# Kernel optimization log

Hardware: AMD Instinct MI355X
Metric: run time of the kernel (lower is better)

Reference implementation:

```python
import jax, jax.numpy as jnp
from jax import lax
import numpy as np

T = 3          # num_frame
DIV = 2        # channel_shift div
PAD = 1        # kernel_size//2 (same padding for k=3)


def setup_inputs() -> dict:
    key = jax.random.key(0)
    k1, k2 = jax.random.split(key)
    x = jax.random.normal(k1, (12, 64, 256, 256), dtype=jnp.float32)      # (B*T, C, H, W)
    weight = jax.random.normal(k2, (64, 64, 3, 3), dtype=jnp.float32)     # (O, I, kh, kw)
    return {"x": x, "weight": weight}


def reference(x, weight):
    BT, C, H, W = x.shape
    B = BT // T
    # channel_shift: view (B, T*C, H, W), roll by C//div along channel axis
    shift = C // DIV
    y = x.reshape(B, T * C, H, W)
    y = jnp.roll(y, shift, axis=1).reshape(BT, C, H, W)
    # BinaryConv2d: sign(activations), sign(weights) * per-out-channel mean|W|
    scale = jnp.mean(jnp.abs(weight), axis=(1, 2, 3), keepdims=True)      # (O,1,1,1)
    bw = jnp.sign(weight) * scale
    bx = jnp.sign(y)
    out = lax.conv_general_dilated(
        bx, bw,
        window_strides=(1, 1),
        padding=[(PAD, PAD), (PAD, PAD)],
        dimension_numbers=("NCHW", "OIHW", "NCHW"),
    )
    return out
```

## Files before the change

### kernel.cpp

```cpp
#include <hip/hip_runtime.h>
#include <stdint.h>

typedef unsigned long long u64;
typedef unsigned int u32;

#define HW 65536
#define WD 256

__global__ __launch_bounds__(64) void pack_w_kernel(const float* __restrict__ wt,
                                                    u64* __restrict__ pw,
                                                    float* __restrict__ scale) {
    const int o = blockIdx.x;
    const int i = threadIdx.x;
    const float* p = wt + o * 576 + i * 9;
    float v[9];
    float s = 0.f;
#pragma unroll
    for (int k = 0; k < 9; k++) { v[k] = p[k]; s += fabsf(v[k]); }
#pragma unroll
    for (int k = 0; k < 9; k++) {
        u64 m = __ballot((__float_as_uint(v[k]) >> 31) != 0u);
        if (i == 0) pw[o * 9 + k] = m;
    }
#pragma unroll
    for (int off = 32; off > 0; off >>= 1) s += __shfl_down(s, off);
    if (i == 0) scale[o] = s * (1.0f / 576.0f);
}

__global__ __launch_bounds__(256) void pack_x_kernel(const float* __restrict__ x,
                                                     u64* __restrict__ px) {
    const int n = blockIdx.x >> 6;
    const int s = ((blockIdx.x & 63) << 10) + (threadIdx.x << 2);
    const int b = n / 3;
    const int t = n - b * 3;
    const int fp = b * 3 + (t + 2) % 3;

    const float* xa = x + ((size_t)fp * 64 + 32) * HW + s;
    const float* xb = x + (size_t)n * 64 * HW + s;

    u32 lo0 = 0, lo1 = 0, lo2 = 0, lo3 = 0;
    u32 hi0 = 0, hi1 = 0, hi2 = 0, hi3 = 0;
#pragma unroll
    for (int c = 0; c < 32; c++) {
        float4 va = *(const float4*)(xa + (size_t)c * HW);
        lo0 |= (__float_as_uint(va.x) >> 31) << c;
        lo1 |= (__float_as_uint(va.y) >> 31) << c;
        lo2 |= (__float_as_uint(va.z) >> 31) << c;
        lo3 |= (__float_as_uint(va.w) >> 31) << c;
        float4 vb = *(const float4*)(xb + (size_t)c * HW);
        hi0 |= (__float_as_uint(vb.x) >> 31) << c;
        hi1 |= (__float_as_uint(vb.y) >> 31) << c;
        hi2 |= (__float_as_uint(vb.z) >> 31) << c;
        hi3 |= (__float_as_uint(vb.w) >> 31) << c;
    }
    u64* dst = px + (size_t)n * HW + s;
    dst[0] = ((u64)hi0 << 32) | lo0;
    dst[1] = ((u64)hi1 << 32) | lo1;
    dst[2] = ((u64)hi2 << 32) | lo2;
    dst[3] = ((u64)hi3 << 32) | lo3;
}

__global__ __launch_bounds__(256) void bconv_kernel(const u64* __restrict__ px,
                                                    const u64* __restrict__ pw,
                                                    const float* __restrict__ scale,
                                                    float* __restrict__ out) {
    const int w = (blockIdx.x << 6) + (threadIdx.x & 63);
    const int h = (blockIdx.y << 2) + (threadIdx.x >> 6);
    const int n = blockIdx.z;
    const u64* base = px + (size_t)n * HW;

    const bool edge_block = (blockIdx.x == 0) | (blockIdx.x == 3) |
                            (blockIdx.y == 0) | (blockIdx.y == 63);

    u64 xv[9];
    float* op = out + (size_t)n * 64 * HW + h * WD + w;

    if (!edge_block) {
#pragma unroll
        for (int dh = -1; dh <= 1; dh++)
#pragma unroll
            for (int dw = -1; dw <= 1; dw++)
                xv[(dh + 1) * 3 + (dw + 1)] = base[(h + dh) * WD + (w + dw)];

#pragma unroll 4
        for (int o = 0; o < 64; o++) {
            const u64* wp = pw + o * 9;
            int cnt = 0;
#pragma unroll
            for (int k = 0; k < 9; k++) cnt += __popcll(xv[k] ^ wp[k]);
            const float sc = scale[o];
            __builtin_nontemporal_store(fmaf(-2.f * sc, (float)cnt, 576.f * sc),
                                        op + (size_t)o * HW);
        }
    } else {
        u64 mk[9];
        int ninv = 0;
#pragma unroll
        for (int dh = -1; dh <= 1; dh++) {
#pragma unroll
            for (int dw = -1; dw <= 1; dw++) {
                const int k = (dh + 1) * 3 + (dw + 1);
                const int hh = h + dh, ww = w + dw;
                const bool valid = (hh >= 0) && (hh < 256) && (ww >= 0) && (ww < 256);
                const int hc = min(max(hh, 0), 255);
                const int wc = min(max(ww, 0), 255);
                xv[k] = base[hc * WD + wc];
                mk[k] = valid ? ~0ull : 0ull;
                ninv += valid ? 0 : 1;
            }
        }
        const int basecnt = 32 * ninv;

#pragma unroll 4
        for (int o = 0; o < 64; o++) {
            const u64* wp = pw + o * 9;
            int cnt = basecnt;
#pragma unroll
            for (int k = 0; k < 9; k++) cnt += __popcll((xv[k] ^ wp[k]) & mk[k]);
            const float sc = scale[o];
            __builtin_nontemporal_store(fmaf(-2.f * sc, (float)cnt, 576.f * sc),
                                        op + (size_t)o * HW);
        }
    }
}

extern "C" void kernel_launch(void* const* d_in, const int* in_sizes, int n_in,
                              void* d_out, int out_size, void* d_ws, size_t ws_size,
                              hipStream_t stream) {
    (void)in_sizes; (void)n_in; (void)out_size; (void)ws_size;
    const float* x  = (const float*)d_in[0];
    const float* wt = (const float*)d_in[1];
    float* out = (float*)d_out;

    u64* px = (u64*)d_ws;
    u64* pw = px + (size_t)12 * HW;
    float* scale = (float*)(pw + 576);

    pack_w_kernel<<<64, 64, 0, stream>>>(wt, pw, scale);
    pack_x_kernel<<<768, 256, 0, stream>>>(x, px);
    bconv_kernel<<<dim3(4, 64, 12), 256, 0, stream>>>(px, pw, scale, out);
}
```

Baseline: 382.7 us.

## Restructure binary conv to one output channel per block with rolling row reuse

The conv kernel now gives each block one (frame, output channel) pair. Each wave sweeps 64 rows of the image with a three-row rolling register window, and each lane computes four adjacent output pixels. Every output row is written as one vectorized float4 nontemporal store, and the padding correction is computed from weight popcounts instead of per-tap masks. The aim is to cut redundant loads of the packed input and scattered scalar stores. In exchange, packed input rows are reloaded once per output channel across 64 blocks, which relies on L2 caching.

New measurement: 393.1 us. +2.7%, slower.

```diff
diff --git a/kernel.cpp b/kernel.cpp
--- a/kernel.cpp
+++ b/kernel.cpp
@@ -3,6 +3,7 @@
 
 typedef unsigned long long u64;
 typedef unsigned int u32;
+typedef float fx4 __attribute__((ext_vector_type(4)));
 
 #define HW 65536
 #define WD 256
@@ -60,68 +61,96 @@
     dst[3] = ((u64)hi3 << 32) | lo3;
 }
 
+struct Row { u64 l, a, b, c, d, r; };
+
+__device__ __forceinline__ void load_row(Row& R, const u64* rp, int w0,
+                                         bool lane0, bool lane63) {
+    ulonglong2 t0 = *(const ulonglong2*)(rp + w0);
+    ulonglong2 t1 = *(const ulonglong2*)(rp + w0 + 2);
+    R.a = t0.x; R.b = t0.y; R.c = t1.x; R.d = t1.y;
+    u64 lv = rp[lane0 ? 0 : (w0 - 1)];
+    u64 rv = rp[lane63 ? 255 : (w0 + 4)];
+    R.l = lane0 ? 0ull : lv;
+    R.r = lane63 ? 0ull : rv;
+}
+
+__device__ __forceinline__ void acc_row(int& c0, int& c1, int& c2, int& c3,
+                                        const Row& R, u64 wl, u64 wm, u64 wr) {
+    c0 += __popcll(R.l ^ wl) + __popcll(R.a ^ wm) + __popcll(R.b ^ wr);
+    c1 += __popcll(R.a ^ wl) + __popcll(R.b ^ wm) + __popcll(R.c ^ wr);
+    c2 += __popcll(R.b ^ wl) + __popcll(R.c ^ wm) + __popcll(R.d ^ wr);
+    c3 += __popcll(R.c ^ wl) + __popcll(R.d ^ wm) + __popcll(R.r ^ wr);
+}
+
 __global__ __launch_bounds__(256) void bconv_kernel(const u64* __restrict__ px,
                                                     const u64* __restrict__ pw,
                                                     const float* __restrict__ scale,
                                                     float* __restrict__ out) {
-    const int w = (blockIdx.x << 6) + (threadIdx.x & 63);
-    const int h = (blockIdx.y << 2) + (threadIdx.x >> 6);
-    const int n = blockIdx.z;
+    const int n = blockIdx.x >> 6;
+    const int o = blockIdx.x & 63;
+    const int lane = threadIdx.x & 63;
+    const int wave = threadIdx.x >> 6;
+    const int w0 = lane << 2;
+    const int r0 = wave << 6;
+    const bool lane0 = (lane == 0);
+    const bool lane63 = (lane == 63);
+
     const u64* base = px + (size_t)n * HW;
 
-    const bool edge_block = (blockIdx.x == 0) | (blockIdx.x == 3) |
-                            (blockIdx.y == 0) | (blockIdx.y == 63);
+    const u64 wv0 = pw[o * 9 + 0], wv1 = pw[o * 9 + 1], wv2 = pw[o * 9 + 2];
+    const u64 wv3 = pw[o * 9 + 3], wv4 = pw[o * 9 + 4], wv5 = pw[o * 9 + 5];
+    const u64 wv6 = pw[o * 9 + 6], wv7 = pw[o * 9 + 7], wv8 = pw[o * 9 + 8];
+    const int pcx0 = 32 - __popcll(wv0), pcx1 = 32 - __popcll(wv1);
+    const int pcx2 = 32 - __popcll(wv2), pcx3 = 32 - __popcll(wv3);
+    const int pcx5 = 32 - __popcll(wv5), pcx6 = 32 - __popcll(wv6);
+    const int pcx7 = 32 - __popcll(wv7), pcx8 = 32 - __popcll(wv8);
+    const int cT = pcx0 + pcx1 + pcx2;
+    const int cB = pcx6 + pcx7 + pcx8;
 
-    u64 xv[9];
-    float* op = out + (size_t)n * 64 * HW + h * WD + w;
+    const float sc = scale[o];
+    const float fa = -2.f * sc, fb = 576.f * sc;
 
-    if (!edge_block) {
-#pragma unroll
-        for (int dh = -1; dh <= 1; dh++)
-#pragma unroll
-            for (int dw = -1; dw <= 1; dw++)
-                xv[(dh + 1) * 3 + (dw + 1)] = base[(h + dh) * WD + (w + dw)];
+    float* op = out + ((size_t)n * 64 + o) * HW;
 
-#pragma unroll 4
-        for (int o = 0; o < 64; o++) {
-            const u64* wp = pw + o * 9;
-            int cnt = 0;
-#pragma unroll
-            for (int k = 0; k < 9; k++) cnt += __popcll(xv[k] ^ wp[k]);
-            const float sc = scale[o];
-            __builtin_nontemporal_store(fmaf(-2.f * sc, (float)cnt, 576.f * sc),
-                                        op + (size_t)o * HW);
-        }
-    } else {
-        u64 mk[9];
-        int ninv = 0;
-#pragma unroll
-        for (int dh = -1; dh <= 1; dh++) {
-#pragma unroll
-            for (int dw = -1; dw <= 1; dw++) {
-                const int k = (dh + 1) * 3 + (dw + 1);
-                const int hh = h + dh, ww = w + dw;
-                const bool valid = (hh >= 0) && (hh < 256) && (ww >= 0) && (ww < 256);
-                const int hc = min(max(hh, 0), 255);
-                const int wc = min(max(ww, 0), 255);
-                xv[k] = base[hc * WD + wc];
-                mk[k] = valid ? ~0ull : 0ull;
-                ninv += valid ? 0 : 1;
-            }
-        }
-        const int basecnt = 32 * ninv;
+    Row A, B, C;
+    if (wave == 0) { A.l = A.a = A.b = A.c = A.d = A.r = 0ull; }
+    else           load_row(A, base + (r0 - 1) * WD, w0, lane0, lane63);
+    load_row(B, base + r0 * WD, w0, lane0, lane63);
+    int r = r0;
 
-#pragma unroll 4
-        for (int o = 0; o < 64; o++) {
-            const u64* wp = pw + o * 9;
-            int cnt = basecnt;
-#pragma unroll
-            for (int k = 0; k < 9; k++) cnt += __popcll((xv[k] ^ wp[k]) & mk[k]);
-            const float sc = scale[o];
-            __builtin_nontemporal_store(fmaf(-2.f * sc, (float)cnt, 576.f * sc),
-                                        op + (size_t)o * HW);
-        }
+#define STEP(A_, B_, C_) {                                                     \
+    const bool va = (r > 0);                                                   \
+    const bool vc = (r < 255);                                                 \
+    if (vc) load_row(C_, base + (r + 1) * WD, w0, lane0, lane63);              \
+    else    { C_.l = C_.a = C_.b = C_.c = C_.d = C_.r = 0ull; }                \
+    const int bc = (va ? 0 : cT) + (vc ? 0 : cB);                              \
+    int c0 = bc, c1 = bc, c2 = bc, c3 = bc;                                    \
+    {                                                                          \
+        const int lc = pcx3 + (va ? pcx0 : 0) + (vc ? pcx6 : 0);               \
+        const int rc = pcx5 + (va ? pcx2 : 0) + (vc ? pcx8 : 0);               \
+        c0 += lane0 ? lc : 0;                                                  \
+        c3 += lane63 ? rc : 0;                                                 \
+    }                                                                          \
+    acc_row(c0, c1, c2, c3, A_, wv0, wv1, wv2);                                \
+    acc_row(c0, c1, c2, c3, B_, wv3, wv4, wv5);                                \
+    acc_row(c0, c1, c2, c3, C_, wv6, wv7, wv8);                                \
+    fx4 v;                                                                     \
+    v.x = fmaf(fa, (float)c0, fb);                                             \
+    v.y = fmaf(fa, (float)c1, fb);                                             \
+    v.z = fmaf(fa, (float)c2, fb);                                             \
+    v.w = fmaf(fa, (float)c3, fb);                                             \
+    __builtin_nontemporal_store(v, (fx4*)(op + (size_t)r * WD + w0));          \
+    r++;                                                                       \
+}
+
+#pragma unroll 1
+    for (int it = 0; it < 21; ++it) {
+        STEP(A, B, C)
+        STEP(B, C, A)
+        STEP(C, A, B)
     }
+    STEP(A, B, C)
+#undef STEP
 }
 
 extern "C" void kernel_launch(void* const* d_in, const int* in_sizes, int n_in,
@@ -138,5 +167,5 @@
 
     pack_w_kernel<<<64, 64, 0, stream>>>(wt, pw, scale);
     pack_x_kernel<<<768, 256, 0, stream>>>(x, px);
-    bconv_kernel<<<dim3(4, 64, 12), 256, 0, stream>>>(px, pw, scale, out);
+    bconv_kernel<<<768, 256, 0, stream>>>(px, pw, scale, out);
 }
```

## Fuse sign-packing of activations into the binary conv kernel via LDS tiles

Applied to the files above, without the earlier changes.

Merges the activation bit-packing pass into the convolution kernel: each block packs a 10x72 halo tile of sign bits into shared memory, then computes an 8x64 output tile from it. This removes the packed-activation round trip through global memory and one kernel launch. The cost is redundant packing of halo rows and columns (about 1.4x reads of the input), fewer threads active during the packing phase, and a barrier between phases.

Result: faster. 374.9 us (-2.0%).

```diff
diff --git a/kernel.cpp b/kernel.cpp
--- a/kernel.cpp
+++ b/kernel.cpp
@@ -27,99 +27,124 @@
     if (i == 0) scale[o] = s * (1.0f / 576.0f);
 }
 
-__global__ __launch_bounds__(256) void pack_x_kernel(const float* __restrict__ x,
-                                                     u64* __restrict__ px) {
-    const int n = blockIdx.x >> 6;
-    const int s = ((blockIdx.x & 63) << 10) + (threadIdx.x << 2);
+#define LROWS 10
+#define LCOLS 72
+#define NGRP  18
+
+__global__ __launch_bounds__(256) void fused_kernel(const float* __restrict__ x,
+                                                    const u64* __restrict__ pw,
+                                                    const float* __restrict__ scale,
+                                                    float* __restrict__ out) {
+    const int tx = blockIdx.x;
+    const int ty = blockIdx.y;
+    const int n  = blockIdx.z;
+    const int gw0 = tx << 6;
+    const int gh0 = ty << 3;
+
     const int b = n / 3;
     const int t = n - b * 3;
     const int fp = b * 3 + (t + 2) % 3;
 
-    const float* xa = x + ((size_t)fp * 64 + 32) * HW + s;
-    const float* xb = x + (size_t)n * 64 * HW + s;
+    const float* xa = x + ((size_t)fp * 64 + 32) * HW;
+    const float* xb = x + (size_t)n * 64 * HW;
 
-    u32 lo0 = 0, lo1 = 0, lo2 = 0, lo3 = 0;
-    u32 hi0 = 0, hi1 = 0, hi2 = 0, hi3 = 0;
+    __shared__ u64 ph[LROWS][LCOLS];
+
+    const int tid = threadIdx.x;
+
+    if (tid < LROWS * NGRP) {
+        const int row = tid / NGRP;
+        const int grp = tid - row * NGRP;
+        const int gh  = gh0 - 1 + row;
+        const int gwb = gw0 - 4 + (grp << 2);
+        u64 w0 = 0, w1 = 0, w2 = 0, w3 = 0;
+        if ((gh >= 0) & (gh < 256) & (gwb >= 0) & (gwb < 256)) {
+            const float* pa = xa + (size_t)gh * WD + gwb;
+            const float* pb = xb + (size_t)gh * WD + gwb;
+            u32 l0 = 0, l1 = 0, l2 = 0, l3 = 0;
+            u32 h0 = 0, h1 = 0, h2 = 0, h3 = 0;
 #pragma unroll
-    for (int c = 0; c < 32; c++) {
-        float4 va = *(const float4*)(xa + (size_t)c * HW);
-        lo0 |= (__float_as_uint(va.x) >> 31) << c;
-        lo1 |= (__float_as_uint(va.y) >> 31) << c;
-        lo2 |= (__float_as_uint(va.z) >> 31) << c;
-        lo3 |= (__float_as_uint(va.w) >> 31) << c;
-        float4 vb = *(const float4*)(xb + (size_t)c * HW);
-        hi0 |= (__float_as_uint(vb.x) >> 31) << c;
-        hi1 |= (__float_as_uint(vb.y) >> 31) << c;
-        hi2 |= (__float_as_uint(vb.z) >> 31) << c;
-        hi3 |= (__float_as_uint(vb.w) >> 31) << c;
+            for (int c = 0; c < 32; c++) {
+                float4 va = *(const float4*)(pa + (size_t)c * HW);
+                l0 |= (__float_as_uint(va.x) >> 31) << c;
+                l1 |= (__float_as_uint(va.y) >> 31) << c;
+                l2 |= (__float_as_uint(va.z) >> 31) << c;
+                l3 |= (__float_as_uint(va.w) >> 31) << c;
+                float4 vb = *(const float4*)(pb + (size_t)c * HW);
+                h0 |= (__float_as_uint(vb.x) >> 31) << c;
+                h1 |= (__float_as_uint(vb.y) >> 31) << c;
+                h2 |= (__float_as_uint(vb.z) >> 31) << c;
+                h3 |= (__float_as_uint(vb.w) >> 31) << c;
+            }
+            w0 = ((u64)h0 << 32) | l0;
+            w1 = ((u64)h1 << 32) | l1;
+            w2 = ((u64)h2 << 32) | l2;
+            w3 = ((u64)h3 << 32) | l3;
+        }
+        const int c0 = grp << 2;
+        ph[row][c0 + 0] = w0;
+        ph[row][c0 + 1] = w1;
+        ph[row][c0 + 2] = w2;
+        ph[row][c0 + 3] = w3;
     }
-    u64* dst = px + (size_t)n * HW + s;
-    dst[0] = ((u64)hi0 << 32) | lo0;
-    dst[1] = ((u64)hi1 << 32) | lo1;
-    dst[2] = ((u64)hi2 << 32) | lo2;
-    dst[3] = ((u64)hi3 << 32) | lo3;
-}
+    __syncthreads();
 
-__global__ __launch_bounds__(256) void bconv_kernel(const u64* __restrict__ px,
-                                                    const u64* __restrict__ pw,
-                                                    const float* __restrict__ scale,
-                                                    float* __restrict__ out) {
-    const int w = (blockIdx.x << 6) + (threadIdx.x & 63);
-    const int h = (blockIdx.y << 2) + (threadIdx.x >> 6);
-    const int n = blockIdx.z;
-    const u64* base = px + (size_t)n * HW;
+    const int q  = tid >> 6;
+    const int w  = tid & 63;
+    const int gw = gw0 + w;
+    const bool edge_block = (tx == 0) | (tx == 3) | (ty == 0) | (ty == 31);
 
-    const bool edge_block = (blockIdx.x == 0) | (blockIdx.x == 3) |
-                            (blockIdx.y == 0) | (blockIdx.y == 63);
+    float* op = out + (size_t)n * 64 * HW + gw;
 
-    u64 xv[9];
-    float* op = out + (size_t)n * 64 * HW + h * WD + w;
+#pragma unroll
+    for (int k = 0; k < 2; k++) {
+        const int hl = q + (k << 2);
+        const int gh = gh0 + hl;
+        u64 xv[9];
+#pragma unroll
+        for (int dr = 0; dr < 3; dr++)
+#pragma unroll
+            for (int dc = 0; dc < 3; dc++)
+                xv[dr * 3 + dc] = ph[hl + dr][w + 3 + dc];
 
-    if (!edge_block) {
+        float* oprow = op + (size_t)gh * WD;
+
+        if (!edge_block) {
+#pragma unroll 4
+            for (int o = 0; o < 64; o++) {
+                const u64* wp = pw + o * 9;
+                int cnt = 0;
 #pragma unroll
-        for (int dh = -1; dh <= 1; dh++)
+                for (int kk = 0; kk < 9; kk++) cnt += __popcll(xv[kk] ^ wp[kk]);
+                const float sc = scale[o];
+                __builtin_nontemporal_store(fmaf(-2.f * sc, (float)cnt, 576.f * sc),
+                                            oprow + (size_t)o * HW);
+            }
+        } else {
+            u64 mk[9];
+            int ninv = 0;
 #pragma unroll
-            for (int dw = -1; dw <= 1; dw++)
-                xv[(dh + 1) * 3 + (dw + 1)] = base[(h + dh) * WD + (w + dw)];
+            for (int dr = -1; dr <= 1; dr++) {
+#pragma unroll
+                for (int dc = -1; dc <= 1; dc++) {
+                    const int hh = gh + dr, ww = gw + dc;
+                    const bool valid = (hh >= 0) && (hh < 256) && (ww >= 0) && (ww < 256);
+                    mk[(dr + 1) * 3 + (dc + 1)] = valid ? ~0ull : 0ull;
+                    ninv += valid ? 0 : 1;
+                }
+            }
+            const int basecnt = 32 * ninv;
 
 #pragma unroll 4
-        for (int o = 0; o < 64; o++) {
-            const u64* wp = pw + o * 9;
-            int cnt = 0;
+            for (int o = 0; o < 64; o++) {
+                const u64* wp = pw + o * 9;
+                int cnt = basecnt;
 #pragma unroll
-            for (int k = 0; k < 9; k++) cnt += __popcll(xv[k] ^ wp[k]);
-            const float sc = scale[o];
-            __builtin_nontemporal_store(fmaf(-2.f * sc, (float)cnt, 576.f * sc),
-                                        op + (size_t)o * HW);
-        }
-    } else {
-        u64 mk[9];
-        int ninv = 0;
-#pragma unroll
-        for (int dh = -1; dh <= 1; dh++) {
-#pragma unroll
-            for (int dw = -1; dw <= 1; dw++) {
-                const int k = (dh + 1) * 3 + (dw + 1);
-                const int hh = h + dh, ww = w + dw;
-                const bool valid = (hh >= 0) && (hh < 256) && (ww >= 0) && (ww < 256);
-                const int hc = min(max(hh, 0), 255);
-                const int wc = min(max(ww, 0), 255);
-                xv[k] = base[hc * WD + wc];
-                mk[k] = valid ? ~0ull : 0ull;
-                ninv += valid ? 0 : 1;
+                for (int kk = 0; kk < 9; kk++) cnt += __popcll((xv[kk] ^ wp[kk]) & mk[kk]);
+                const float sc = scale[o];
+                __builtin_nontemporal_store(fmaf(-2.f * sc, (float)cnt, 576.f * sc),
+                                            oprow + (size_t)o * HW);
             }
-        }
-        const int basecnt = 32 * ninv;
-
-#pragma unroll 4
-        for (int o = 0; o < 64; o++) {
-            const u64* wp = pw + o * 9;
-            int cnt = basecnt;
-#pragma unroll
-            for (int k = 0; k < 9; k++) cnt += __popcll((xv[k] ^ wp[k]) & mk[k]);
-            const float sc = scale[o];
-            __builtin_nontemporal_store(fmaf(-2.f * sc, (float)cnt, 576.f * sc),
-                                        op + (size_t)o * HW);
         }
     }
 }
@@ -132,11 +157,9 @@
     const float* wt = (const float*)d_in[1];
     float* out = (float*)d_out;
 
-    u64* px = (u64*)d_ws;
-    u64* pw = px + (size_t)12 * HW;
+    u64* pw = (u64*)d_ws;
     float* scale = (float*)(pw + 576);
 
     pack_w_kernel<<<64, 64, 0, stream>>>(wt, pw, scale);
-    pack_x_kernel<<<768, 256, 0, stream>>>(x, px);
-    bconv_kernel<<<dim3(4, 64, 12), 256, 0, stream>>>(px, pw, scale, out);
+    fused_kernel<<<dim3(4, 32, 12), 256, 0, stream>>>(x, pw, scale, out);
 }
```

## Replace popcount binary conv with int8 MFMA over zero-padded ±1 tensors

Applied to the files above, without the earlier changes.

Activations and weights are now packed as int8 ±1 values into a zero-padded (258x258x64) layout, and the convolution runs as int8 MFMA 16x16x64 over the 9 taps instead of XOR/popcount on 64-bit masks. The explicit padding removes the edge-case masking path. The cost is an 8x larger packed activation buffer (more memory traffic for packing and reading) and an extra zeroing kernel. Output stores are no longer nontemporal, and the store pattern now has lanes writing 16 consecutive floats per output channel.

New measurement: 434.7 us. +13.6%, slower.

```diff
diff --git a/kernel.cpp b/kernel.cpp
--- a/kernel.cpp
+++ b/kernel.cpp
@@ -3,123 +3,144 @@
 
 typedef unsigned long long u64;
 typedef unsigned int u32;
+typedef int i32x4 __attribute__((ext_vector_type(4)));
 
 #define HW 65536
 #define WD 256
+#define ROWB (258 * 64)
+#define RS (258 * ROWB)
 
-__global__ __launch_bounds__(64) void pack_w_kernel(const float* __restrict__ wt,
-                                                    u64* __restrict__ pw,
-                                                    float* __restrict__ scale) {
+__global__ __launch_bounds__(64) void pack_w2(const float* __restrict__ wt,
+                                              char* __restrict__ sw,
+                                              float* __restrict__ scale) {
     const int o = blockIdx.x;
-    const int i = threadIdx.x;
-    const float* p = wt + o * 576 + i * 9;
-    float v[9];
+    const int c = threadIdx.x;
+    const float* p = wt + o * 576 + c * 9;
     float s = 0.f;
 #pragma unroll
-    for (int k = 0; k < 9; k++) { v[k] = p[k]; s += fabsf(v[k]); }
-#pragma unroll
     for (int k = 0; k < 9; k++) {
-        u64 m = __ballot((__float_as_uint(v[k]) >> 31) != 0u);
-        if (i == 0) pw[o * 9 + k] = m;
+        const u32 u = __float_as_uint(p[k]);
+        s += fabsf(p[k]);
+        sw[k * 4096 + o * 64 + c] = (char)(1 + (((int)u >> 31) & 0xFE));
     }
 #pragma unroll
     for (int off = 32; off > 0; off >>= 1) s += __shfl_down(s, off);
-    if (i == 0) scale[o] = s * (1.0f / 576.0f);
+    if (c == 0) scale[o] = s * (1.0f / 576.0f);
 }
 
-__global__ __launch_bounds__(256) void pack_x_kernel(const float* __restrict__ x,
-                                                     u64* __restrict__ px) {
-    const int n = blockIdx.x >> 6;
-    const int s = ((blockIdx.x & 63) << 10) + (threadIdx.x << 2);
+__global__ __launch_bounds__(320) void zero_tb(char* __restrict__ sx) {
+    const int n = blockIdx.x >> 1;
+    const int row = (blockIdx.x & 1) * 257;
+    const int t = threadIdx.x;
+    if (t < 258) {
+        uint4 z = make_uint4(0, 0, 0, 0);
+        uint4* d = (uint4*)(sx + (size_t)n * RS + (size_t)row * ROWB + t * 64);
+        d[0] = z; d[1] = z; d[2] = z; d[3] = z;
+    }
+}
+
+__global__ __launch_bounds__(256) void pack_x2(const float* __restrict__ x,
+                                               char* __restrict__ sx) {
+    const int band = blockIdx.x;
+    const int n = blockIdx.y;
+    const int wv = threadIdx.x >> 6;
+    const int lane = threadIdx.x & 63;
+    const int r = (band << 2) + wv;
+
     const int b = n / 3;
     const int t = n - b * 3;
     const int fp = b * 3 + (t + 2) % 3;
 
-    const float* xa = x + ((size_t)fp * 64 + 32) * HW + s;
-    const float* xb = x + (size_t)n * 64 * HW + s;
+    const float* xa = x + ((size_t)fp * 64 + 32) * HW + r * WD + (lane << 2);
+    const float* xb = x + (size_t)n * 64 * HW + r * WD + (lane << 2);
 
-    u32 lo0 = 0, lo1 = 0, lo2 = 0, lo3 = 0;
-    u32 hi0 = 0, hi1 = 0, hi2 = 0, hi3 = 0;
+    char* dstrow = sx + (size_t)n * RS + (size_t)(r + 1) * ROWB;
+
 #pragma unroll
-    for (int c = 0; c < 32; c++) {
-        float4 va = *(const float4*)(xa + (size_t)c * HW);
-        lo0 |= (__float_as_uint(va.x) >> 31) << c;
-        lo1 |= (__float_as_uint(va.y) >> 31) << c;
-        lo2 |= (__float_as_uint(va.z) >> 31) << c;
-        lo3 |= (__float_as_uint(va.w) >> 31) << c;
-        float4 vb = *(const float4*)(xb + (size_t)c * HW);
-        hi0 |= (__float_as_uint(vb.x) >> 31) << c;
-        hi1 |= (__float_as_uint(vb.y) >> 31) << c;
-        hi2 |= (__float_as_uint(vb.z) >> 31) << c;
-        hi3 |= (__float_as_uint(vb.w) >> 31) << c;
+    for (int cc = 0; cc < 4; cc++) {
+        const float* base = (cc < 2) ? (xa + (size_t)(cc * 16) * HW)
+                                     : (xb + (size_t)((cc - 2) * 16) * HW);
+        u32 w0[4] = {0, 0, 0, 0}, w1[4] = {0, 0, 0, 0};
+        u32 w2[4] = {0, 0, 0, 0}, w3[4] = {0, 0, 0, 0};
+#pragma unroll
+        for (int ci = 0; ci < 16; ci++) {
+            float4 v = *(const float4*)(base + (size_t)ci * HW);
+            const int sh = (ci & 3) * 8;
+            const int wi = ci >> 2;
+            w0[wi] |= (1u + ((u32)((int)__float_as_uint(v.x) >> 31) & 0xFEu)) << sh;
+            w1[wi] |= (1u + ((u32)((int)__float_as_uint(v.y) >> 31) & 0xFEu)) << sh;
+            w2[wi] |= (1u + ((u32)((int)__float_as_uint(v.z) >> 31) & 0xFEu)) << sh;
+            w3[wi] |= (1u + ((u32)((int)__float_as_uint(v.w) >> 31) & 0xFEu)) << sh;
+        }
+        char* d = dstrow + (size_t)((lane << 2) + 1) * 64 + cc * 16;
+        *(uint4*)(d)       = make_uint4(w0[0], w0[1], w0[2], w0[3]);
+        *(uint4*)(d + 64)  = make_uint4(w1[0], w1[1], w1[2], w1[3]);
+        *(uint4*)(d + 128) = make_uint4(w2[0], w2[1], w2[2], w2[3]);
+        *(uint4*)(d + 192) = make_uint4(w3[0], w3[1], w3[2], w3[3]);
     }
-    u64* dst = px + (size_t)n * HW + s;
-    dst[0] = ((u64)hi0 << 32) | lo0;
-    dst[1] = ((u64)hi1 << 32) | lo1;
-    dst[2] = ((u64)hi2 << 32) | lo2;
-    dst[3] = ((u64)hi3 << 32) | lo3;
+
+    if (threadIdx.x < 8) {
+        const int rr = (band << 2) + (threadIdx.x >> 1) + 1;
+        const int col = (threadIdx.x & 1) * 257;
+        uint4 z = make_uint4(0, 0, 0, 0);
+        uint4* d = (uint4*)(sx + (size_t)n * RS + (size_t)rr * ROWB + (size_t)col * 64);
+        d[0] = z; d[1] = z; d[2] = z; d[3] = z;
+    }
 }
 
-__global__ __launch_bounds__(256) void bconv_kernel(const u64* __restrict__ px,
-                                                    const u64* __restrict__ pw,
+__global__ __launch_bounds__(256, 2) void conv_mfma(const char* __restrict__ sx,
+                                                    const char* __restrict__ sw,
                                                     const float* __restrict__ scale,
                                                     float* __restrict__ out) {
-    const int w = (blockIdx.x << 6) + (threadIdx.x & 63);
-    const int h = (blockIdx.y << 2) + (threadIdx.x >> 6);
-    const int n = blockIdx.z;
-    const u64* base = px + (size_t)n * HW;
+    const int bx = blockIdx.x;
+    const int n = blockIdx.y;
+    const int gh = ((bx & 7) << 5) | (bx >> 3);
+    const int lane = threadIdx.x & 63;
+    const int wv = threadIdx.x >> 6;
+    const int lr = lane & 15;
+    const int q = lane >> 4;
 
-    const bool edge_block = (blockIdx.x == 0) | (blockIdx.x == 3) |
-                            (blockIdx.y == 0) | (blockIdx.y == 63);
+    i32x4 a[4][9];
+#pragma unroll
+    for (int og = 0; og < 4; og++)
+#pragma unroll
+        for (int tap = 0; tap < 9; tap++)
+            a[og][tap] = *(const i32x4*)(sw + (size_t)(tap * 64 + og * 16 + lr) * 64 + q * 16);
 
-    u64 xv[9];
-    float* op = out + (size_t)n * 64 * HW + h * WD + w;
+    float sc[4][4];
+#pragma unroll
+    for (int og = 0; og < 4; og++)
+#pragma unroll
+        for (int reg = 0; reg < 4; reg++)
+            sc[og][reg] = scale[og * 16 + q * 4 + reg];
 
-    if (!edge_block) {
+    const char* sxn = sx + (size_t)n * RS;
+    float* ob = out + (size_t)n * 64 * HW + gh * WD;
+    const int px0w = wv << 6;
+
 #pragma unroll
-        for (int dh = -1; dh <= 1; dh++)
+    for (int pxg = 0; pxg < 4; pxg++) {
+        const int px0 = px0w + (pxg << 4);
+        i32x4 bfr[9];
 #pragma unroll
-            for (int dw = -1; dw <= 1; dw++)
-                xv[(dh + 1) * 3 + (dw + 1)] = base[(h + dh) * WD + (w + dw)];
+        for (int tr = 0; tr < 3; tr++)
+#pragma unroll
+            for (int tc = 0; tc < 3; tc++)
+                bfr[tr * 3 + tc] = *(const i32x4*)(sxn
+                    + (size_t)(gh + tr) * ROWB
+                    + (size_t)(px0 + lr + tc) * 64 + q * 16);
 
-#pragma unroll 4
-        for (int o = 0; o < 64; o++) {
-            const u64* wp = pw + o * 9;
-            int cnt = 0;
 #pragma unroll
-            for (int k = 0; k < 9; k++) cnt += __popcll(xv[k] ^ wp[k]);
-            const float sc = scale[o];
-            __builtin_nontemporal_store(fmaf(-2.f * sc, (float)cnt, 576.f * sc),
-                                        op + (size_t)o * HW);
-        }
-    } else {
-        u64 mk[9];
-        int ninv = 0;
+        for (int og = 0; og < 4; og++) {
+            i32x4 acc = {0, 0, 0, 0};
 #pragma unroll
-        for (int dh = -1; dh <= 1; dh++) {
+            for (int tap = 0; tap < 9; tap++)
+                acc = __builtin_amdgcn_mfma_i32_16x16x64_i8(a[og][tap], bfr[tap], acc, 0, 0, 0);
 #pragma unroll
-            for (int dw = -1; dw <= 1; dw++) {
-                const int k = (dh + 1) * 3 + (dw + 1);
-                const int hh = h + dh, ww = w + dw;
-                const bool valid = (hh >= 0) && (hh < 256) && (ww >= 0) && (ww < 256);
-                const int hc = min(max(hh, 0), 255);
-                const int wc = min(max(ww, 0), 255);
-                xv[k] = base[hc * WD + wc];
-                mk[k] = valid ? ~0ull : 0ull;
-                ninv += valid ? 0 : 1;
+            for (int reg = 0; reg < 4; reg++) {
+                const int o = og * 16 + q * 4 + reg;
+                ob[(size_t)o * HW + px0 + lr] = sc[og][reg] * (float)acc[reg];
             }
-        }
-        const int basecnt = 32 * ninv;
-
-#pragma unroll 4
-        for (int o = 0; o < 64; o++) {
-            const u64* wp = pw + o * 9;
-            int cnt = basecnt;
-#pragma unroll
-            for (int k = 0; k < 9; k++) cnt += __popcll((xv[k] ^ wp[k]) & mk[k]);
-            const float sc = scale[o];
-            __builtin_nontemporal_store(fmaf(-2.f * sc, (float)cnt, 576.f * sc),
-                                        op + (size_t)o * HW);
         }
     }
 }
@@ -132,11 +153,12 @@
     const float* wt = (const float*)d_in[1];
     float* out = (float*)d_out;
 
-    u64* px = (u64*)d_ws;
-    u64* pw = px + (size_t)12 * HW;
-    float* scale = (float*)(pw + 576);
+    char* sx = (char*)d_ws;
+    char* sw = sx + (size_t)12 * RS;
+    float* scale = (float*)(sw + 9 * 4096);
 
-    pack_w_kernel<<<64, 64, 0, stream>>>(wt, pw, scale);
-    pack_x_kernel<<<768, 256, 0, stream>>>(x, px);
-    bconv_kernel<<<dim3(4, 64, 12), 256, 0, stream>>>(px, pw, scale, out);
+    pack_w2<<<64, 64, 0, stream>>>(wt, sw, scale);
+    zero_tb<<<24, 320, 0, stream>>>(sx);
+    pack_x2<<<dim3(64, 12), 256, 0, stream>>>(x, sx);
+    conv_mfma<<<dim3(256, 12), 256, 0, stream>>>(sx, sw, scale, out);
 }
```
